# Kernel optimization log

Hardware: AMD Instinct MI355X
Metric: run time of the kernel (lower is better)

The kernel has to match this reference:

```python
import jax, jax.numpy as jnp
import numpy as np

B, W, L = 32768, 5, 20            # batch, words per example, max chars per word
WV, CV = 50000, 100               # word vocab, char vocab
CE, OC, K = 32, 30, 3             # char embed dim, conv out channels (=window_size), kernel
WE, HID, TAGS = 50, 100, 36       # word embed dim, fc1 hidden, output tags


def setup_inputs() -> dict:
    key = jax.random.key(0)
    ks = jax.random.split(key, 8)
    inp = jax.random.randint(ks[0], (B, W, 1 + L), 0, 100, dtype=jnp.int32)
    embedding_matrix = jax.random.normal(ks[1], (WV, WE), jnp.float32).at[0].set(0.0)  # padding_idx=0, frozen
    char_emb = jax.random.normal(ks[2], (CV, CE), jnp.float32).at[0].set(0.0)          # padding_idx=0
    conv_w = jax.random.normal(ks[3], (OC, CE, K), jnp.float32) * 0.1
    conv_b = jnp.zeros((OC,), jnp.float32)
    fc1_w = jax.random.normal(ks[4], (HID, (WE + OC) * W), jnp.float32) * 0.05
    fc1_b = jnp.zeros((HID,), jnp.float32)
    out_w = jax.random.normal(ks[5], (TAGS, HID), jnp.float32) * 0.1
    out_b = jnp.zeros((TAGS,), jnp.float32)
    return dict(input=inp, embedding_matrix=embedding_matrix, char_emb=char_emb,
                conv_w=conv_w, conv_b=conv_b, fc1_w=fc1_w, fc1_b=fc1_b,
                out_w=out_w, out_b=out_b)


def reference(input, embedding_matrix, char_emb, conv_w, conv_b, fc1_w, fc1_b, out_w, out_b):
    b = input.shape[0]
    word_ids = input[:, :, 0]                 # [B, W]
    char_ids = input[:, :, 1:]                # [B, W, L]
    we = embedding_matrix[word_ids]           # [B, W, 50]
    ce = char_emb[char_ids]                   # [B, W, L, CE]
    # conv1d over char axis, batched over all B*W words at once
    x = ce.reshape(b * W, L, CE).transpose(0, 2, 1)        # [B*W, CE, L]
    conv = jax.lax.conv_general_dilated(
        x, conv_w, window_strides=(1,), padding='VALID',
        dimension_numbers=('NCH', 'OIH', 'NCH')) + conv_b[None, :, None]  # [B*W, OC, L-2]
    pooled = conv.max(axis=2).reshape(b, W, OC)            # max pool over time
    feats = jnp.concatenate([we, pooled], axis=-1).reshape(b, -1)  # [B, (50+OC)*W]
    h = jnp.tanh(feats @ fc1_w.T + fc1_b)     # dropout is a no-op at inference
    return h @ out_w.T + out_b                # [B, 36]
```

## Files before the change

kernel.cpp:

```cpp
#include <hip/hip_runtime.h>

#define B_TOT 32768
#define OC 30
#define HID 100
#define TAGS 36

#define NI 16
#define FS 212
#define HS 68

#define WS_TH  0
#define WS_FC1 6000
#define WS_OUT 29296

typedef __attribute__((ext_vector_type(8))) _Float16 half8;
typedef __attribute__((ext_vector_type(2))) _Float16 h2v;
typedef __attribute__((ext_vector_type(4))) float f32x4;

__device__ inline half8 ash8(uint4 u) {
    union { uint4 a; half8 b; } v; v.a = u; return v.b;
}
__device__ inline unsigned int h2u(h2v h) {
    union { h2v a; unsigned int b; } v; v.a = h; return v.b;
}
__device__ inline h2v u2h(unsigned int u) {
    union { unsigned int a; h2v b; } v; v.a = u; return v.b;
}
__device__ inline unsigned int pk_f16(float a, float b) {
    h2v h; h.x = (_Float16)a; h.y = (_Float16)b; return h2u(h);
}

__global__ void prep(const float* __restrict__ conv_w,
                     const float* __restrict__ char_emb,
                     const float* __restrict__ fc1_w,
                     const float* __restrict__ out_w,
                     unsigned int* __restrict__ ws) {
    int idx = blockIdx.x * 256 + threadIdx.x;
    if (idx < 6000) {
        int rd = idx % 20, row = idx / 20;
        int c = row % 100, k = row / 100;
        float v[2];
        #pragma unroll
        for (int e = 0; e < 2; ++e) {
            int oc = rd * 2 + e;
            float s = 0.f;
            if (oc < OC) {
                for (int ce = 0; ce < 32; ++ce)
                    s += char_emb[c * 32 + ce] * conv_w[(oc * 32 + ce) * 3 + k];
            }
            v[e] = s;
        }
        ws[WS_TH + idx] = pk_f16(v[0], v[1]);
    } else if (idx < 6000 + 23296) {
        int t = idx - 6000;
        int dw = t & 3, lane = (t >> 2) & 63, chunk = t >> 8;
        int ks = chunk % 13, nt = chunk / 13;
        int j = nt * 16 + (lane & 15);
        int k = ks * 32 + (lane >> 4) * 8 + dw * 2;
        float a = (j < HID && k     < 400) ? fc1_w[j * 400 + k]     : 0.f;
        float b = (j < HID && k + 1 < 400) ? fc1_w[j * 400 + k + 1] : 0.f;
        ws[WS_FC1 + t] = pk_f16(a, b);
    } else if (idx < 29296 + 3072) {
        int t = idx - 29296;
        int dw = t & 3, lane = (t >> 2) & 63, chunk = t >> 8;
        int ks = chunk % 4, nt = chunk / 4;
        int j = nt * 16 + (lane & 15);
        int k = ks * 32 + (lane >> 4) * 8 + dw * 2;
        float a = (j < TAGS && k     < HID) ? out_w[j * 100 + k]     : 0.f;
        float b = (j < TAGS && k + 1 < HID) ? out_w[j * 100 + k + 1] : 0.f;
        ws[WS_OUT + t] = pk_f16(a, b);
    }
}

__global__ __launch_bounds__(256)
void pos_fused(const int*   __restrict__ input,
               const float* __restrict__ emb,
               const float* __restrict__ conv_b,
               const float* __restrict__ fc1_b,
               const float* __restrict__ out_b,
               const unsigned int* __restrict__ ws,
               float*       __restrict__ out)
{
    __shared__ unsigned int Ths[6000];
    __shared__ unsigned int F[NI * FS];
    __shared__ int          ids[NI * 105];
    __shared__ unsigned int Hh[NI * HS];

    const int tid   = threadIdx.x;
    const int item0 = blockIdx.x * NI;

    for (int idx = tid; idx < 6000; idx += 256) Ths[idx] = ws[WS_TH + idx];
    const int* inp = input + item0 * 105;
    for (int idx = tid; idx < NI * 105; idx += 256) ids[idx] = inp[idx];
    for (int idx = tid; idx < NI * 12; idx += 256) F[(idx / 12) * FS + 200 + idx % 12] = 0;
    for (int idx = tid; idx < NI * 18; idx += 256) Hh[(idx / 18) * HS + 50 + idx % 18] = 0;
    __syncthreads();

    for (int idx = tid; idx < NI * 5 * 25; idx += 256) {
        int ph = idx % 25;
        int w  = (idx / 25) % 5;
        int i  = idx / 125;
        int wid = ids[i * 105 + w * 21];
        float2 e = *(const float2*)&emb[wid * 50 + ph * 2];
        F[i * FS + w * 40 + ph] = pk_f16(e.x, e.y);
    }

    {
        const int q4  = tid & 3;
        const int grp = tid >> 2;
        const int oc0 = q4 * 8;
        h2v bias[4];
        #pragma unroll
        for (int d = 0; d < 4; ++d) {
            int a = oc0 + 2 * d, b = a + 1;
            bias[d].x = (_Float16)(a < OC ? conv_b[a] : 0.f);
            bias[d].y = (_Float16)(b < OC ? conv_b[b] : 0.f);
        }
        for (int task = grp; task < NI * 5; task += 64) {
            int i = task / 5, w = task % 5;
            const int* cp = &ids[i * 105 + w * 21 + 1];
            int c[20];
            #pragma unroll
            for (int p = 0; p < 20; ++p) c[p] = cp[p];
            h2v m[4];
            #pragma unroll
            for (int d = 0; d < 4; ++d) { m[d].x = (_Float16)(-30000.f); m[d].y = (_Float16)(-30000.f); }
            #pragma unroll 6
            for (int p = 0; p < 18; ++p) {
                uint4 ra = *(const uint4*)&Ths[c[p    ] * 20        + q4 * 4];
                uint4 rb = *(const uint4*)&Ths[c[p + 1] * 20 + 2000 + q4 * 4];
                uint4 rc = *(const uint4*)&Ths[c[p + 2] * 20 + 4000 + q4 * 4];
                unsigned int* pa = (unsigned int*)&ra;
                unsigned int* pb = (unsigned int*)&rb;
                unsigned int* pc = (unsigned int*)&rc;
                #pragma unroll
                for (int d = 0; d < 4; ++d) {
                    h2v s = u2h(pa[d]) + u2h(pb[d]) + u2h(pc[d]);
                    m[d] = __builtin_elementwise_max(m[d], s);
                }
            }
            int base = i * FS + w * 40 + 25 + q4 * 4;
            F[base]     = h2u(m[0] + bias[0]);
            F[base + 1] = h2u(m[1] + bias[1]);
            F[base + 2] = h2u(m[2] + bias[2]);
            if (q4 < 3) F[base + 3] = h2u(m[3] + bias[3]);
        }
    }
    __syncthreads();

    const int wv   = tid >> 6;
    const int lane = tid & 63;
    const int ln15 = lane & 15;
    const int quad = lane >> 4;
    {
        const int nt0 = wv * 2;
        const int NT  = (wv < 3) ? 2 : 1;
        f32x4 acc[2] = {f32x4{0,0,0,0}, f32x4{0,0,0,0}};
        const uint4* wp = (const uint4*)(ws + WS_FC1);
        const int aoff = ln15 * FS + quad * 4;
        for (int ks = 0; ks < 13; ++ks) {
            half8 a = ash8(*(const uint4*)&F[aoff + ks * 16]);
            #pragma unroll
            for (int t = 0; t < 2; ++t) {
                if (t < NT) {
                    uint4 bv = wp[((nt0 + t) * 13 + ks) * 64 + lane];
                    acc[t] = __builtin_amdgcn_mfma_f32_16x16x32_f16(a, ash8(bv), acc[t], 0, 0, 0);
                }
            }
        }
        #pragma unroll
        for (int t = 0; t < 2; ++t) {
            if (t < NT) {
                int j = (nt0 + t) * 16 + ln15;
                if (j < HID) {
                    float bj = fc1_b[j];
                    #pragma unroll
                    for (int r = 0; r < 4; ++r) {
                        int it = quad * 4 + r;
                        float hv = tanhf(acc[t][r] + bj);
                        _Float16 h = (_Float16)hv;
                        ((unsigned short*)Hh)[it * (HS * 2) + j] =
                            *reinterpret_cast<unsigned short*>(&h);
                    }
                }
            }
        }
    }
    __syncthreads();

    if (wv < 3) {
        f32x4 acc = f32x4{0, 0, 0, 0};
        const uint4* wp = (const uint4*)(ws + WS_OUT);
        const int aoff = ln15 * HS + quad * 4;
        #pragma unroll
        for (int ks = 0; ks < 4; ++ks) {
            half8 a = ash8(*(const uint4*)&Hh[aoff + ks * 16]);
            uint4 bv = wp[(wv * 4 + ks) * 64 + lane];
            acc = __builtin_amdgcn_mfma_f32_16x16x32_f16(a, ash8(bv), acc, 0, 0, 0);
        }
        int o = wv * 16 + ln15;
        if (o < TAGS) {
            float bo = out_b[o];
            #pragma unroll
            for (int r = 0; r < 4; ++r) {
                int it = item0 + quad * 4 + r;
                out[it * TAGS + o] = acc[r] + bo;
            }
        }
    }
}

extern "C" void kernel_launch(void* const* d_in, const int* in_sizes, int n_in,
                              void* d_out, int out_size, void* d_ws, size_t ws_size,
                              hipStream_t stream) {
    const int*   input  = (const int*)  d_in[0];
    const float* emb    = (const float*)d_in[1];
    const float* char_e = (const float*)d_in[2];
    const float* conv_w = (const float*)d_in[3];
    const float* conv_b = (const float*)d_in[4];
    const float* fc1_w  = (const float*)d_in[5];
    const float* fc1_b  = (const float*)d_in[6];
    const float* out_w  = (const float*)d_in[7];
    const float* out_b  = (const float*)d_in[8];
    unsigned int* ws = (unsigned int*)d_ws;

    prep<<<127, 256, 0, stream>>>(conv_w, char_e, fc1_w, out_w, ws);
    pos_fused<<<B_TOT / NI, 256, 0, stream>>>(input, emb, conv_b, fc1_b, out_b,
                                              ws, (float*)d_out);
}
```

Baseline: 135.6 us.

## Make each wave own 16 items end-to-end, removing block barriers

Each block now handles 64 items, with every wave processing its own 16 items through embedding gather, char conv, fc1 and output layers in a private LDS slice. This removes the intra-block __syncthreads between stages and amortizes the 24KB Ths table load over four times as many items. Char ids are read directly from global memory instead of being staged in shared memory. The trade-off is that each wave now issues all 7 fc1 weight tiles and 3 output tiles itself, which raises register pressure and global weight traffic per wave. Launch bounds now request 2 blocks per CU.

```diff
diff --git a/kernel.cpp b/kernel.cpp
--- a/kernel.cpp
+++ b/kernel.cpp
@@ -4,10 +4,6 @@
 #define OC 30
 #define HID 100
 #define TAGS 36
-
-#define NI 16
-#define FS 212
-#define HS 68
 
 #define WS_TH  0
 #define WS_FC1 6000
@@ -72,7 +68,7 @@
     }
 }
 
-__global__ __launch_bounds__(256)
+__global__ __launch_bounds__(256, 2)
 void pos_fused(const int*   __restrict__ input,
                const float* __restrict__ emb,
                const float* __restrict__ conv_b,
@@ -82,32 +78,40 @@
                float*       __restrict__ out)
 {
     __shared__ unsigned int Ths[6000];
-    __shared__ unsigned int F[NI * FS];
-    __shared__ int          ids[NI * 105];
-    __shared__ unsigned int Hh[NI * HS];
-
-    const int tid   = threadIdx.x;
-    const int item0 = blockIdx.x * NI;
+    __shared__ unsigned int F[4][16 * 212];
+
+    const int tid  = threadIdx.x;
+    const int wv   = tid >> 6;
+    const int lane = tid & 63;
+    const int ln15 = lane & 15;
+    const int quad = lane >> 4;
+    const int item0 = blockIdx.x * 64 + wv * 16;
+    unsigned int* Fw = &F[wv][0];
 
     for (int idx = tid; idx < 6000; idx += 256) Ths[idx] = ws[WS_TH + idx];
-    const int* inp = input + item0 * 105;
-    for (int idx = tid; idx < NI * 105; idx += 256) ids[idx] = inp[idx];
-    for (int idx = tid; idx < NI * 12; idx += 256) F[(idx / 12) * FS + 200 + idx % 12] = 0;
-    for (int idx = tid; idx < NI * 18; idx += 256) Hh[(idx / 18) * HS + 50 + idx % 18] = 0;
     __syncthreads();
 
-    for (int idx = tid; idx < NI * 5 * 25; idx += 256) {
-        int ph = idx % 25;
-        int w  = (idx / 25) % 5;
-        int i  = idx / 125;
-        int wid = ids[i * 105 + w * 21];
-        float2 e = *(const float2*)&emb[wid * 50 + ph * 2];
-        F[i * FS + w * 40 + ph] = pk_f16(e.x, e.y);
-    }
-
-    {
-        const int q4  = tid & 3;
-        const int grp = tid >> 2;
+    {
+        int i = lane >> 2, d0 = 200 + (lane & 3) * 2;
+        Fw[i * 212 + d0]     = 0;
+        Fw[i * 212 + d0 + 1] = 0;
+    }
+
+    for (int t = 0; t < 32; ++t) {
+        int idx = t * 64 + lane;
+        if (idx < 2000) {
+            int ph = idx % 25;
+            int w  = (idx / 25) % 5;
+            int i  = idx / 125;
+            int wid = input[(item0 + i) * 105 + w * 21];
+            float2 e = *(const float2*)&emb[wid * 50 + ph * 2];
+            Fw[i * 212 + w * 40 + ph] = pk_f16(e.x, e.y);
+        }
+    }
+
+    {
+        const int q4  = lane & 3;
+        const int grp = lane >> 2;
         const int oc0 = q4 * 8;
         h2v bias[4];
         #pragma unroll
@@ -116,9 +120,11 @@
             bias[d].x = (_Float16)(a < OC ? conv_b[a] : 0.f);
             bias[d].y = (_Float16)(b < OC ? conv_b[b] : 0.f);
         }
-        for (int task = grp; task < NI * 5; task += 64) {
+        #pragma unroll
+        for (int round = 0; round < 5; ++round) {
+            int task = round * 16 + grp;
             int i = task / 5, w = task % 5;
-            const int* cp = &ids[i * 105 + w * 21 + 1];
+            const int* cp = &input[(item0 + i) * 105 + w * 21 + 1];
             int c[20];
             #pragma unroll
             for (int p = 0; p < 20; ++p) c[p] = cp[p];
@@ -139,72 +145,77 @@
                     m[d] = __builtin_elementwise_max(m[d], s);
                 }
             }
-            int base = i * FS + w * 40 + 25 + q4 * 4;
-            F[base]     = h2u(m[0] + bias[0]);
-            F[base + 1] = h2u(m[1] + bias[1]);
-            F[base + 2] = h2u(m[2] + bias[2]);
-            if (q4 < 3) F[base + 3] = h2u(m[3] + bias[3]);
-        }
-    }
-    __syncthreads();
-
-    const int wv   = tid >> 6;
-    const int lane = tid & 63;
-    const int ln15 = lane & 15;
-    const int quad = lane >> 4;
-    {
-        const int nt0 = wv * 2;
-        const int NT  = (wv < 3) ? 2 : 1;
-        f32x4 acc[2] = {f32x4{0,0,0,0}, f32x4{0,0,0,0}};
+            int base = i * 212 + w * 40 + 25 + q4 * 4;
+            Fw[base]     = h2u(m[0] + bias[0]);
+            Fw[base + 1] = h2u(m[1] + bias[1]);
+            Fw[base + 2] = h2u(m[2] + bias[2]);
+            if (q4 < 3) Fw[base + 3] = h2u(m[3] + bias[3]);
+        }
+    }
+
+    f32x4 acc[7];
+    #pragma unroll
+    for (int t = 0; t < 7; ++t) acc[t] = f32x4{0, 0, 0, 0};
+    {
         const uint4* wp = (const uint4*)(ws + WS_FC1);
-        const int aoff = ln15 * FS + quad * 4;
+        const int aoff = ln15 * 212 + quad * 4;
         for (int ks = 0; ks < 13; ++ks) {
-            half8 a = ash8(*(const uint4*)&F[aoff + ks * 16]);
-            #pragma unroll
-            for (int t = 0; t < 2; ++t) {
-                if (t < NT) {
-                    uint4 bv = wp[((nt0 + t) * 13 + ks) * 64 + lane];
-                    acc[t] = __builtin_amdgcn_mfma_f32_16x16x32_f16(a, ash8(bv), acc[t], 0, 0, 0);
+            half8 a = ash8(*(const uint4*)&Fw[aoff + ks * 16]);
+            #pragma unroll
+            for (int t = 0; t < 7; ++t) {
+                uint4 bv = wp[(t * 13 + ks) * 64 + lane];
+                acc[t] = __builtin_amdgcn_mfma_f32_16x16x32_f16(a, ash8(bv), acc[t], 0, 0, 0);
+            }
+        }
+    }
+
+    {
+        for (int t2 = lane; t2 < 224; t2 += 64) {
+            int i = t2 / 14, d = t2 % 14;
+            Fw[i * 68 + 50 + d] = 0;
+        }
+        unsigned short* Hw = (unsigned short*)Fw;
+        #pragma unroll
+        for (int t = 0; t < 7; ++t) {
+            int j = t * 16 + ln15;
+            if (j < HID) {
+                float bj = fc1_b[j];
+                #pragma unroll
+                for (int r = 0; r < 4; ++r) {
+                    int it = quad * 4 + r;
+                    float hv = tanhf(acc[t][r] + bj);
+                    _Float16 h = (_Float16)hv;
+                    Hw[it * 136 + j] = *reinterpret_cast<unsigned short*>(&h);
                 }
             }
         }
-        #pragma unroll
-        for (int t = 0; t < 2; ++t) {
-            if (t < NT) {
-                int j = (nt0 + t) * 16 + ln15;
-                if (j < HID) {
-                    float bj = fc1_b[j];
-                    #pragma unroll
-                    for (int r = 0; r < 4; ++r) {
-                        int it = quad * 4 + r;
-                        float hv = tanhf(acc[t][r] + bj);
-                        _Float16 h = (_Float16)hv;
-                        ((unsigned short*)Hh)[it * (HS * 2) + j] =
-                            *reinterpret_cast<unsigned short*>(&h);
-                    }
+    }
+
+    {
+        f32x4 oacc[3];
+        #pragma unroll
+        for (int t = 0; t < 3; ++t) oacc[t] = f32x4{0, 0, 0, 0};
+        const uint4* wpo = (const uint4*)(ws + WS_OUT);
+        const int aoff2 = ln15 * 68 + quad * 4;
+        #pragma unroll
+        for (int ks = 0; ks < 4; ++ks) {
+            half8 a = ash8(*(const uint4*)&Fw[aoff2 + ks * 16]);
+            #pragma unroll
+            for (int t = 0; t < 3; ++t) {
+                uint4 bv = wpo[(t * 4 + ks) * 64 + lane];
+                oacc[t] = __builtin_amdgcn_mfma_f32_16x16x32_f16(a, ash8(bv), oacc[t], 0, 0, 0);
+            }
+        }
+        #pragma unroll
+        for (int t = 0; t < 3; ++t) {
+            int o = t * 16 + ln15;
+            if (o < TAGS) {
+                float bo = out_b[o];
+                #pragma unroll
+                for (int r = 0; r < 4; ++r) {
+                    int it = item0 + quad * 4 + r;
+                    out[it * TAGS + o] = oacc[t][r] + bo;
                 }
-            }
-        }
-    }
-    __syncthreads();
-
-    if (wv < 3) {
-        f32x4 acc = f32x4{0, 0, 0, 0};
-        const uint4* wp = (const uint4*)(ws + WS_OUT);
-        const int aoff = ln15 * HS + quad * 4;
-        #pragma unroll
-        for (int ks = 0; ks < 4; ++ks) {
-            half8 a = ash8(*(const uint4*)&Hh[aoff + ks * 16]);
-            uint4 bv = wp[(wv * 4 + ks) * 64 + lane];
-            acc = __builtin_amdgcn_mfma_f32_16x16x32_f16(a, ash8(bv), acc, 0, 0, 0);
-        }
-        int o = wv * 16 + ln15;
-        if (o < TAGS) {
-            float bo = out_b[o];
-            #pragma unroll
-            for (int r = 0; r < 4; ++r) {
-                int it = item0 + quad * 4 + r;
-                out[it * TAGS + o] = acc[r] + bo;
             }
         }
     }
@@ -225,6 +236,6 @@
     unsigned int* ws = (unsigned int*)d_ws;
 
     prep<<<127, 256, 0, stream>>>(conv_w, char_e, fc1_w, out_w, ws);
-    pos_fused<<<B_TOT / NI, 256, 0, stream>>>(input, emb, conv_b, fc1_b, out_b,
+    pos_fused<<<B_TOT / 64, 256, 0, stream>>>(input, emb, conv_b, fc1_b, out_b,
                                               ws, (float*)d_out);
 }
```

Result: faster. 127.9 us (-5.7%).
